# Kernel optimization log

Hardware: AMD Instinct MI355X
Metric: run time of the kernel (lower is better)

## Reference

```python
import jax, jax.numpy as jnp
import numpy as np

N_NODES = 100000
N_EDGES = 3200000
N_CLASSES = 16
P = 2  # p-norm order


def setup_inputs() -> dict:
    key = jax.random.key(0)
    k1, k2, k3 = jax.random.split(key, 3)
    edge_index = jax.random.randint(k1, (2, N_EDGES), 0, N_NODES, dtype=jnp.int64)
    edge_weights = jax.random.uniform(k2, (N_EDGES,), dtype=jnp.float32)
    y = jax.random.normal(k3, (N_NODES, N_CLASSES), dtype=jnp.float32)
    return {"edge_index": edge_index, "edge_weights": edge_weights, "y": y}


def reference(edge_index, edge_weights, y):
    row, col = edge_index[0], edge_index[1]
    n = y.shape[0]
    # sym normalization: degree = row-sum of weighted adjacency (O(E) segment sum,
    # replacing the original dense NxN materialization)
    degree = jax.ops.segment_sum(edge_weights, row, num_segments=n)
    d = jnp.sqrt(degree)
    d_r = d[row][:, None]  # (E,1)
    d_c = d[col][:, None]
    diff = y[row] / d_r - y[col] / d_c  # (E,C)
    pnorm = jnp.sum(jnp.abs(diff) ** P, axis=1) ** (1.0 / P)  # (E,)
    return jnp.mean(pnorm * edge_weights)
```

## Files before the change

kernel.cpp:

```cpp
#include <hip/hip_runtime.h>
#include <hip/hip_fp16.h>

#define N_NODES   100000
#define N_CLASSES 16
#define N_EDGES   3200000

#define R5        5
#define NPR5      20000
#define DYN5      (NPR5 * 4)
#define S5        102
#define EPS5      31376

#define R_ST      8
#define NPR_ST    12500
#define S_ST      64
#define EPS_ST    50000

#define B_DEG     1024
#define KE        8


__device__ __forceinline__ unsigned f2fp8(float f) {
    unsigned u = __float_as_uint(f);
    unsigned s = (u >> 24) & 0x80u;
    float g = fabsf(f) * 0x1p-120f;
    unsigned gu = __float_as_uint(g);
    gu += 0x7FFFFu + ((gu >> 20) & 1u);
    unsigned mag = gu >> 20;
    if (mag > 0x7Eu) mag = 0x7Eu;
    return s | mag;
}

__device__ __forceinline__ float fp82f(unsigned b) {
    unsigned u = ((b & 0x80u) << 24) | ((b & 0x7Fu) << 20);
    return __uint_as_float(u) * 0x1p120f;
}

#if defined(__has_builtin)
#if __has_builtin(__builtin_amdgcn_cvt_pk_f32_fp8)
#define HAVE_HW_FP8 1
#endif
#endif

#ifdef HAVE_HW_FP8
typedef float v2f __attribute__((ext_vector_type(2)));
__device__ __forceinline__ float ssd4(unsigned a, unsigned b) {
    v2f a0 = __builtin_amdgcn_cvt_pk_f32_fp8((int)a, false);
    v2f a1 = __builtin_amdgcn_cvt_pk_f32_fp8((int)a, true);
    v2f b0 = __builtin_amdgcn_cvt_pk_f32_fp8((int)b, false);
    v2f b1 = __builtin_amdgcn_cvt_pk_f32_fp8((int)b, true);
    float d0 = a0.x - b0.x;
    float d1 = a0.y - b0.y;
    float d2 = a1.x - b1.x;
    float d3 = a1.y - b1.y;
    return d0 * d0 + d1 * d1 + d2 * d2 + d3 * d3;
}
#else
__device__ __forceinline__ float ssd4(unsigned a, unsigned b) {
    float s = 0.0f;
#pragma unroll
    for (int i = 0; i < 4; ++i) {
        float va = fp82f((a >> (8 * i)) & 0xFFu);
        float vb = fp82f((b >> (8 * i)) & 0xFFu);
        float d = va - vb;
        s += d * d;
    }
    return s;
}
#endif


__global__ __launch_bounds__(B_DEG, 8) void lap_degree_r5(
        const int* __restrict__ rows, const float* __restrict__ w,
        __half* __restrict__ shadows, float* __restrict__ out) {
    extern __shared__ float hist[];
    const int b  = blockIdx.x;
    const int r  = b % R5;
    const int s  = b / R5;
    const int lo = r * NPR5;

    if (b == 0 && threadIdx.x == 0) out[0] = 0.0f;

    for (int i = threadIdx.x; i < NPR5; i += B_DEG) hist[i] = 0.0f;
    __syncthreads();

    const int base = s * EPS5;
    for (int g = threadIdx.x; g < EPS5 / 4; g += B_DEG) {
        const int e = base + g * 4;
        if (e >= N_EDGES) continue;
        int4   r4 = *(const int4*)(rows + e);
        float4 w4 = *(const float4*)(w + e);
        int t;
        t = r4.x - lo; if ((unsigned)t < (unsigned)NPR5) atomicAdd(&hist[t], w4.x);
        t = r4.y - lo; if ((unsigned)t < (unsigned)NPR5) atomicAdd(&hist[t], w4.y);
        t = r4.z - lo; if ((unsigned)t < (unsigned)NPR5) atomicAdd(&hist[t], w4.z);
        t = r4.w - lo; if ((unsigned)t < (unsigned)NPR5) atomicAdd(&hist[t], w4.w);
    }
    __syncthreads();

    __half* dst = shadows + (size_t)s * N_NODES + lo;
    for (int i = threadIdx.x; i < NPR5; i += B_DEG) dst[i] = __float2half(hist[i]);
}


__global__ __launch_bounds__(B_DEG) void lap_degree_static(
        const int* __restrict__ rows, const float* __restrict__ w,
        __half* __restrict__ shadows, float* __restrict__ out) {
    __shared__ float hist[NPR_ST];
    const int r  = blockIdx.x & (R_ST - 1);
    const int s  = blockIdx.x >> 3;
    const int lo = r * NPR_ST;

    if (blockIdx.x == 0 && threadIdx.x == 0) out[0] = 0.0f;

    for (int i = threadIdx.x; i < NPR_ST; i += B_DEG) hist[i] = 0.0f;
    __syncthreads();

    const int base = s * EPS_ST;
    for (int g = threadIdx.x; g < EPS_ST / 4; g += B_DEG) {
        const int e = base + g * 4;
        int4   r4 = *(const int4*)(rows + e);
        float4 w4 = *(const float4*)(w + e);
        int t;
        t = r4.x - lo; if ((unsigned)t < (unsigned)NPR_ST) atomicAdd(&hist[t], w4.x);
        t = r4.y - lo; if ((unsigned)t < (unsigned)NPR_ST) atomicAdd(&hist[t], w4.y);
        t = r4.z - lo; if ((unsigned)t < (unsigned)NPR_ST) atomicAdd(&hist[t], w4.z);
        t = r4.w - lo; if ((unsigned)t < (unsigned)NPR_ST) atomicAdd(&hist[t], w4.w);
    }
    __syncthreads();

    __half* dst = shadows + (size_t)s * N_NODES + lo;
    for (int i = threadIdx.x; i < NPR_ST; i += B_DEG) dst[i] = __float2half(hist[i]);
}


__global__ __launch_bounds__(256) void lap_yhat_par(
        const __half* __restrict__ shadows,
        const float* __restrict__ y,
        unsigned char* __restrict__ yhat, int S) {
    const int lane = threadIdx.x & 63;
    const int wv   = threadIdx.x >> 6;
    const int n    = blockIdx.x * 64 + lane;

    float a0 = 0.0f, a1 = 0.0f, a2 = 0.0f, a3 = 0.0f;
    if (n < N_NODES) {
        const __half* p = shadows + n;
        int s = wv;
        for (; s + 12 < S; s += 16) {
            a0 += __half2float(p[(size_t)(s)      * N_NODES]);
            a1 += __half2float(p[(size_t)(s + 4)  * N_NODES]);
            a2 += __half2float(p[(size_t)(s + 8)  * N_NODES]);
            a3 += __half2float(p[(size_t)(s + 12) * N_NODES]);
        }
        for (; s < S; s += 4)
            a0 += __half2float(p[(size_t)s * N_NODES]);
    }

    __shared__ float sm[4][64];
    sm[wv][lane] = (a0 + a1) + (a2 + a3);
    __syncthreads();

    if (wv == 0 && n < N_NODES) {
        const float deg = (sm[0][lane] + sm[1][lane]) + (sm[2][lane] + sm[3][lane]);
        const float inv = rsqrtf(deg);
        const float4* yr = (const float4*)(y + (size_t)n * N_CLASSES);
        uint4 o;
        unsigned* op = (unsigned*)&o;
#pragma unroll
        for (int j = 0; j < 4; ++j) {
            float4 v = yr[j];
            op[j] =  f2fp8(v.x * inv)
                  | (f2fp8(v.y * inv) << 8)
                  | (f2fp8(v.z * inv) << 16)
                  | (f2fp8(v.w * inv) << 24);
        }
        *(uint4*)(yhat + (size_t)n * N_CLASSES) = o;
    }
}


__global__ void lap_edge_fp8(const int* __restrict__ rows,
                             const int* __restrict__ cols,
                             const float* __restrict__ w,
                             const unsigned char* __restrict__ yhat,
                             float* __restrict__ out) {
    const int tid = blockIdx.x * blockDim.x + threadIdx.x;
    const long e0 = (long)tid * KE;
    float local = 0.0f;
    if (e0 < N_EDGES) {
        int4   ra = *(const int4*)(rows + e0);
        int4   rb = *(const int4*)(rows + e0 + 4);
        int4   ca = *(const int4*)(cols + e0);
        int4   cb = *(const int4*)(cols + e0 + 4);
        float4 wa = *(const float4*)(w + e0);
        float4 wb = *(const float4*)(w + e0 + 4);

        const int ri[KE] = {ra.x, ra.y, ra.z, ra.w, rb.x, rb.y, rb.z, rb.w};
        const int ci[KE] = {ca.x, ca.y, ca.z, ca.w, cb.x, cb.y, cb.z, cb.w};
        const float wv[KE] = {wa.x, wa.y, wa.z, wa.w, wb.x, wb.y, wb.z, wb.w};

        uint4 A[KE], B[KE];
#pragma unroll
        for (int k = 0; k < KE; ++k) {
            A[k] = *(const uint4*)(yhat + (size_t)ri[k] * N_CLASSES);
            B[k] = *(const uint4*)(yhat + (size_t)ci[k] * N_CLASSES);
        }
#pragma unroll
        for (int k = 0; k < KE; ++k) {
            float s = ssd4(A[k].x, B[k].x) + ssd4(A[k].y, B[k].y)
                    + ssd4(A[k].z, B[k].z) + ssd4(A[k].w, B[k].w);
            local += wv[k] * sqrtf(s);
        }
    }
#pragma unroll
    for (int off = 32; off > 0; off >>= 1) local += __shfl_down(local, off, 64);
    __shared__ float sm[4];
    const int lane = threadIdx.x & 63;
    const int wid  = threadIdx.x >> 6;
    if (lane == 0) sm[wid] = local;
    __syncthreads();
    if (threadIdx.x == 0)
        atomicAdd(out, (sm[0] + sm[1] + sm[2] + sm[3]) * (1.0f / (float)N_EDGES));
}


__global__ void lap_degree_kernel(const int* __restrict__ rows,
                                  const float* __restrict__ w,
                                  float* __restrict__ degree) {
    int i = blockIdx.x * blockDim.x + threadIdx.x;
    if (i < N_EDGES) atomicAdd(&degree[rows[i]], w[i]);
}

__global__ void lap_invd_kernel(const float* __restrict__ degree,
                                float* __restrict__ invd) {
    int i = blockIdx.x * blockDim.x + threadIdx.x;
    if (i < N_NODES) invd[i] = rsqrtf(degree[i]);
}

__global__ void lap_edge_kernel(const int* __restrict__ rows,
                                const int* __restrict__ cols,
                                const float* __restrict__ w,
                                const float* __restrict__ y,
                                const float* __restrict__ invd,
                                float* __restrict__ out) {
    int i = blockIdx.x * blockDim.x + threadIdx.x;
    float local = 0.0f;
    if (i < N_EDGES) {
        int r = rows[i], c = cols[i];
        float dr = invd[r], dc = invd[c];
        const float4* yr = (const float4*)(y + (size_t)r * N_CLASSES);
        const float4* yc = (const float4*)(y + (size_t)c * N_CLASSES);
        float s = 0.0f;
#pragma unroll
        for (int j = 0; j < N_CLASSES / 4; ++j) {
            float4 a = yr[j], b = yc[j];
            float d0 = a.x * dr - b.x * dc;
            float d1 = a.y * dr - b.y * dc;
            float d2 = a.z * dr - b.z * dc;
            float d3 = a.w * dr - b.w * dc;
            s += d0 * d0 + d1 * d1 + d2 * d2 + d3 * d3;
        }
        local = w[i] * sqrtf(s);
    }
#pragma unroll
    for (int off = 32; off > 0; off >>= 1) local += __shfl_down(local, off, 64);
    __shared__ float sm[4];
    int lane = threadIdx.x & 63, wid = threadIdx.x >> 6;
    if (lane == 0) sm[wid] = local;
    __syncthreads();
    if (threadIdx.x == 0)
        atomicAdd(out, (sm[0] + sm[1] + sm[2] + sm[3]) * (1.0f / (float)N_EDGES));
}


extern "C" void kernel_launch(void* const* d_in, const int* in_sizes, int n_in,
                              void* d_out, int out_size, void* d_ws, size_t ws_size,
                              hipStream_t stream) {
    const int*   edge_index = (const int*)d_in[0];
    const float* w          = (const float*)d_in[1];
    const float* y          = (const float*)d_in[2];
    float*       out        = (float*)d_out;

    const int* rows = edge_index;
    const int* cols = edge_index + N_EDGES;
    const int  B = 256;

    const size_t sh_bytes   = (size_t)S5 * N_NODES * sizeof(__half);
    const size_t need_super = sh_bytes + (size_t)N_NODES * N_CLASSES;

    const int edge_blocks = (N_EDGES / KE + B - 1) / B;
    const int yhat_blocks = (N_NODES + 63) / 64;

    if (ws_size >= need_super) {
        __half*        shadows = (__half*)d_ws;
        unsigned char* yhat    = (unsigned char*)d_ws + sh_bytes;

        hipError_t ok = hipFuncSetAttribute(
            reinterpret_cast<const void*>(lap_degree_r5),
            hipFuncAttributeMaxDynamicSharedMemorySize, DYN5);

        if (ok == hipSuccess) {
            lap_degree_r5<<<R5 * S5, B_DEG, DYN5, stream>>>(rows, w, shadows, out);
            lap_yhat_par<<<yhat_blocks, B, 0, stream>>>(shadows, y, yhat, S5);
        } else {
            lap_degree_static<<<R_ST * S_ST, B_DEG, 0, stream>>>(rows, w, shadows, out);
            lap_yhat_par<<<yhat_blocks, B, 0, stream>>>(shadows, y, yhat, S_ST);
        }
        lap_edge_fp8<<<edge_blocks, B, 0, stream>>>(rows, cols, w, yhat, out);
    } else {
        float* degree = (float*)d_ws;
        float* invd   = degree + N_NODES;
        hipMemsetAsync(d_out, 0, sizeof(float), stream);
        hipMemsetAsync(d_ws, 0, (size_t)N_NODES * sizeof(float), stream);
        lap_degree_kernel<<<(N_EDGES + B - 1) / B, B, 0, stream>>>(rows, w, degree);
        lap_invd_kernel<<<(N_NODES + B - 1) / B, B, 0, stream>>>(degree, invd);
        lap_edge_kernel<<<(N_EDGES + B - 1) / B, B, 0, stream>>>(rows, cols, w, y, invd, out);
    }
}
```

Before: 140.9 us.

## Use packed fp16 LDS atomics for degree histogram with fewer row ranges

Switches the per-block degree histogram from fp32 LDS atomics to packed fp16 ds_pk_add_f16 through inline asm. This halves LDS footprint, so each block covers 50000 nodes and the node space splits into 2 ranges instead of 5. Each edge chunk is therefore scanned only twice, and the shadows are written with 16-byte vector stores. The cost is accumulating each partial degree in fp16, which loses precision, and a shadow buffer with 128 slices.

```diff
diff --git a/kernel.cpp b/kernel.cpp
--- a/kernel.cpp
+++ b/kernel.cpp
@@ -5,11 +5,11 @@
 #define N_CLASSES 16
 #define N_EDGES   3200000
 
-#define R5        5
-#define NPR5      20000
-#define DYN5      (NPR5 * 4)
-#define S5        102
-#define EPS5      31376
+#define R2        2
+#define NPR2      50000
+#define DYN2      (NPR2 * 2)
+#define S2        128
+#define EPS2      25000
 
 #define R_ST      8
 #define NPR_ST    12500
@@ -70,36 +70,45 @@
 #endif
 
 
-__global__ __launch_bounds__(B_DEG, 8) void lap_degree_r5(
+__device__ __forceinline__ void pk_hist_add(unsigned lds_base, int t, float wv) {
+    const unsigned hb   = (unsigned)__half_as_ushort(__float2half(wv));
+    const unsigned data = (t & 1) ? (hb << 16) : hb;
+    const unsigned addr = lds_base + (unsigned)(t >> 1) * 4u;
+    asm volatile("ds_pk_add_f16 %0, %1" :: "v"(addr), "v"(data) : "memory");
+}
+
+__global__ __launch_bounds__(B_DEG) void lap_degree_r2(
         const int* __restrict__ rows, const float* __restrict__ w,
         __half* __restrict__ shadows, float* __restrict__ out) {
-    extern __shared__ float hist[];
+    extern __shared__ __align__(16) unsigned char histb[];
     const int b  = blockIdx.x;
-    const int r  = b % R5;
-    const int s  = b / R5;
-    const int lo = r * NPR5;
+    const int s  = b & (S2 - 1);
+    const int r  = b >> 7;
+    const int lo = r * NPR2;
+    const unsigned lds_base = (unsigned)(size_t)histb;
 
     if (b == 0 && threadIdx.x == 0) out[0] = 0.0f;
 
-    for (int i = threadIdx.x; i < NPR5; i += B_DEG) hist[i] = 0.0f;
-    __syncthreads();
-
-    const int base = s * EPS5;
-    for (int g = threadIdx.x; g < EPS5 / 4; g += B_DEG) {
+    uint4* h4 = (uint4*)histb;
+    for (int i = threadIdx.x; i < DYN2 / 16; i += B_DEG)
+        h4[i] = make_uint4(0u, 0u, 0u, 0u);
+    __syncthreads();
+
+    const int base = s * EPS2;
+    for (int g = threadIdx.x; g < EPS2 / 4; g += B_DEG) {
         const int e = base + g * 4;
-        if (e >= N_EDGES) continue;
         int4   r4 = *(const int4*)(rows + e);
         float4 w4 = *(const float4*)(w + e);
         int t;
-        t = r4.x - lo; if ((unsigned)t < (unsigned)NPR5) atomicAdd(&hist[t], w4.x);
-        t = r4.y - lo; if ((unsigned)t < (unsigned)NPR5) atomicAdd(&hist[t], w4.y);
-        t = r4.z - lo; if ((unsigned)t < (unsigned)NPR5) atomicAdd(&hist[t], w4.z);
-        t = r4.w - lo; if ((unsigned)t < (unsigned)NPR5) atomicAdd(&hist[t], w4.w);
-    }
-    __syncthreads();
-
-    __half* dst = shadows + (size_t)s * N_NODES + lo;
-    for (int i = threadIdx.x; i < NPR5; i += B_DEG) dst[i] = __float2half(hist[i]);
+        t = r4.x - lo; if ((unsigned)t < (unsigned)NPR2) pk_hist_add(lds_base, t, w4.x);
+        t = r4.y - lo; if ((unsigned)t < (unsigned)NPR2) pk_hist_add(lds_base, t, w4.y);
+        t = r4.z - lo; if ((unsigned)t < (unsigned)NPR2) pk_hist_add(lds_base, t, w4.z);
+        t = r4.w - lo; if ((unsigned)t < (unsigned)NPR2) pk_hist_add(lds_base, t, w4.w);
+    }
+    __syncthreads();
+
+    uint4* dst = (uint4*)(shadows + (size_t)s * N_NODES + lo);
+    for (int i = threadIdx.x; i < DYN2 / 16; i += B_DEG) dst[i] = h4[i];
 }
 
 
@@ -285,7 +294,7 @@
     const int* cols = edge_index + N_EDGES;
     const int  B = 256;
 
-    const size_t sh_bytes   = (size_t)S5 * N_NODES * sizeof(__half);
+    const size_t sh_bytes   = (size_t)S2 * N_NODES * sizeof(__half);
     const size_t need_super = sh_bytes + (size_t)N_NODES * N_CLASSES;
 
     const int edge_blocks = (N_EDGES / KE + B - 1) / B;
@@ -296,12 +305,12 @@
         unsigned char* yhat    = (unsigned char*)d_ws + sh_bytes;
 
         hipError_t ok = hipFuncSetAttribute(
-            reinterpret_cast<const void*>(lap_degree_r5),
-            hipFuncAttributeMaxDynamicSharedMemorySize, DYN5);
+            reinterpret_cast<const void*>(lap_degree_r2),
+            hipFuncAttributeMaxDynamicSharedMemorySize, DYN2);
 
         if (ok == hipSuccess) {
-            lap_degree_r5<<<R5 * S5, B_DEG, DYN5, stream>>>(rows, w, shadows, out);
-            lap_yhat_par<<<yhat_blocks, B, 0, stream>>>(shadows, y, yhat, S5);
+            lap_degree_r2<<<R2 * S2, B_DEG, DYN2, stream>>>(rows, w, shadows, out);
+            lap_yhat_par<<<yhat_blocks, B, 0, stream>>>(shadows, y, yhat, S2);
         } else {
             lap_degree_static<<<R_ST * S_ST, B_DEG, 0, stream>>>(rows, w, shadows, out);
             lap_yhat_par<<<yhat_blocks, B, 0, stream>>>(shadows, y, yhat, S_ST);
```

Result: no change. 139.6 us (-0.9%).
